# Optimization experiments

Measured on AMD Instinct MI355X. Metric: run time of the kernel, lower is better.

## Reference

```python
import jax, jax.numpy as jnp
import numpy as np

B = 16384      # batch size
D = 512        # state_dim (= number of graph nodes)
HID = 512      # hidden_dim of main GCN blocks
EH = 32        # hidden dim of ENSO GCN blocks
K = 2          # fourier_modes
OMEGA = 2.0 * np.pi / 12.0


def setup_inputs() -> dict:
    ks = jax.random.split(jax.random.key(0), 20)
    def w(k, shape, scale=0.05):
        return (jax.random.normal(k, shape) * scale).astype(jnp.float32)
    inp = {
        "x": jax.random.normal(ks[0], (B, D), dtype=jnp.float32),
        "t": jax.random.uniform(ks[1], (1,), dtype=jnp.float32) * 12.0,
        "fourier_coeffs": w(ks[2], (D, D, 2 * K + 1), 0.1),
        # quadratic_graph: GCN(D->HID) -> ReLU -> GCN(HID->D)
        "quad_W1": w(ks[3], (D, HID)), "quad_b1": jnp.zeros((HID,), jnp.float32),
        "quad_W2": w(ks[4], (HID, D)), "quad_b2": jnp.zeros((D,), jnp.float32),
        # cubic_graph
        "cubic_W1": w(ks[5], (D, HID)), "cubic_b1": jnp.zeros((HID,), jnp.float32),
        "cubic_W2": w(ks[6], (HID, D)), "cubic_b2": jnp.zeros((D,), jnp.float32),
        # enso_T_graph: GCN(5->32) -> ReLU -> GCN(32->1)
        "ensoT_W1": w(ks[7], (5, EH)), "ensoT_b1": jnp.zeros((EH,), jnp.float32),
        "ensoT_W2": w(ks[8], (EH, 1)), "ensoT_b2": jnp.zeros((1,), jnp.float32),
        # enso_H_graph
        "ensoH_W1": w(ks[9], (5, EH)), "ensoH_b1": jnp.zeros((EH,), jnp.float32),
        "ensoH_W2": w(ks[10], (EH, 1)), "ensoH_b2": jnp.zeros((1,), jnp.float32),
    }
    return inp


def _gcn2(feat, W1, b1, W2, b2):
    # Fully-connected graph + self-loops => normalized adjacency P = (1/N) 11^T.
    # All node rows are identical (x expanded over nodes), so P @ X == X and every
    # node's output is identical: the 2-layer GCN collapses to two dense GEMMs.
    h = jax.nn.relu(feat @ W1 + b1)
    return h @ W2 + b2


def reference(x, t, fourier_coeffs,
              quad_W1, quad_b1, quad_W2, quad_b2,
              cubic_W1, cubic_b1, cubic_W2, cubic_b2,
              ensoT_W1, ensoT_b1, ensoT_W2, ensoT_b2,
              ensoH_W1, ensoH_b1, ensoH_W2, ensoH_b2):
    ts = t[0]
    # --- Seasonal linear operator L(t) = C0 + sum_k Ck^c cos(k w t) + Ck^s sin(k w t)
    L = fourier_coeffs[:, :, 0]
    for k in range(1, K + 1):
        L = L + fourier_coeffs[:, :, 2 * k - 1] * jnp.cos(k * OMEGA * ts)
        L = L + fourier_coeffs[:, :, 2 * k] * jnp.sin(k * OMEGA * ts)
    linear_term = jnp.einsum('ij,bj->bi', L, x)  # [B, D]

    # --- Graph nonlinear terms (per-node outputs identical; mean over feature dim)
    quad = _gcn2(x, quad_W1, quad_b1, quad_W2, quad_b2)        # [B, D]
    cubic = _gcn2(x, cubic_W1, cubic_b1, cubic_W2, cubic_b2)   # [B, D]
    # torch: out[node] identical for all nodes; .mean(dim=1) over features -> same
    # scalar replicated across the state dimension.
    quad_terms = jnp.broadcast_to(quad.mean(axis=1, keepdims=True), (x.shape[0], D))
    cubic_terms = jnp.broadcast_to(cubic.mean(axis=1, keepdims=True), (x.shape[0], D))
    nonlinear = quad_terms + cubic_terms

    # --- ENSO-specific physics (state_dim >= 2)
    T = x[:, 0:1]
    H = x[:, 1:2]
    fT = jnp.concatenate([T, H, T * T, T * H, T * T * T], axis=1)   # [B, 5]
    fH = jnp.concatenate([T, H, T * T, T * H, T * H * H], axis=1)   # [B, 5]
    cT = _gcn2(fT, ensoT_W1, ensoT_b1, ensoT_W2, ensoT_b2)  # [B, 1]
    cH = _gcn2(fH, ensoH_W1, ensoH_b1, ensoH_W2, ensoH_b2)  # [B, 1]
    pad = jnp.zeros((x.shape[0], D - 2), dtype=x.dtype)
    nonlinear = nonlinear + jnp.concatenate([cT, cH, pad], axis=1)

    return linear_term + nonlinear
```

## Files before the change

kernel.cpp:

```cpp
#include <hip/hip_runtime.h>


#define OMEGA_F 0.5235987755982988f

typedef __attribute__((ext_vector_type(8))) short short8;
typedef __attribute__((ext_vector_type(4))) float f32x4;

__device__ __forceinline__ unsigned short f2bf(float f) {
  union { float f; unsigned int u; } a;
  a.f = f;
  unsigned int u = a.u;
  return (unsigned short)((u + 0x7fffu + ((u >> 16) & 1u)) >> 16);
}

__global__ void build_wcat(const float* __restrict__ fc, const float* __restrict__ qW1,
                           const float* __restrict__ cW1, const float* __restrict__ t,
                           unsigned short* __restrict__ WT) {
  int idx = blockIdx.x * 256 + threadIdx.x;
  int n = idx >> 9;
  int k = idx & 511;
  float v;
  if (n < 512) {
    float th = OMEGA_F * t[0];
    float s1, c1, s2, c2;
    sincosf(th, &s1, &c1);
    sincosf(2.0f * th, &s2, &c2);
    const float* p = fc + ((size_t)n * 512 + k) * 5;
    v = p[0] + p[1] * c1 + p[2] * s1 + p[3] * c2 + p[4] * s2;
  } else if (n < 1024) {
    v = qW1[(size_t)k * 512 + (n - 512)];
  } else {
    v = cW1[(size_t)k * 512 + (n - 1024)];
  }
  WT[idx] = f2bf(v);
}

__global__ void build_means(const float* __restrict__ qW2, const float* __restrict__ cW2,
                            const float* __restrict__ qb2, const float* __restrict__ cb2,
                            float* __restrict__ qw2m, float* __restrict__ cw2m,
                            float* __restrict__ b2m) {
  int b = blockIdx.x, tdx = threadIdx.x;
  if (b < 4) {
    const float* W = (b < 2) ? qW2 : cW2;
    float* o = (b < 2) ? qw2m : cw2m;
    int h = (b & 1) * 256 + tdx;
    const float4* row = (const float4*)(W + (size_t)h * 512);
    float s = 0.f;
    for (int i = 0; i < 128; ++i) { float4 v = row[i]; s += (v.x + v.y) + (v.z + v.w); }
    o[h] = s * (1.0f / 512.0f);
  } else {
    __shared__ float sm[256];
    sm[tdx] = qb2[tdx] + qb2[tdx + 256];
    __syncthreads();
    for (int w = 128; w > 0; w >>= 1) { if (tdx < w) sm[tdx] += sm[tdx + w]; __syncthreads(); }
    if (tdx == 0) b2m[0] = sm[0] * (1.0f / 512.0f);
    __syncthreads();
    sm[tdx] = cb2[tdx] + cb2[tdx + 256];
    __syncthreads();
    for (int w = 128; w > 0; w >>= 1) { if (tdx < w) sm[tdx] += sm[tdx + w]; __syncthreads(); }
    if (tdx == 0) b2m[1] = sm[0] * (1.0f / 512.0f);
  }
}

__global__ void enso_kernel(const float* __restrict__ x,
                            const float* __restrict__ tW1, const float* __restrict__ tb1,
                            const float* __restrict__ tW2, const float* __restrict__ tb2,
                            const float* __restrict__ hW1, const float* __restrict__ hb1,
                            const float* __restrict__ hW2, const float* __restrict__ hb2,
                            float* __restrict__ cT, float* __restrict__ cH) {
  int b = blockIdx.x * 256 + threadIdx.x;
  float T = x[(size_t)b * 512];
  float H = x[(size_t)b * 512 + 1];
  float fT[5] = {T, H, T * T, T * H, T * T * T};
  float fH[5] = {T, H, T * T, T * H, T * H * H};
  float sT = tb2[0], sH = hb2[0];
#pragma unroll 4
  for (int e = 0; e < 32; ++e) {
    float a1 = tb1[e], a2 = hb1[e];
#pragma unroll
    for (int f = 0; f < 5; ++f) {
      a1 += fT[f] * tW1[f * 32 + e];
      a2 += fH[f] * hW1[f * 32 + e];
    }
    sT += fmaxf(a1, 0.f) * tW2[e];
    sH += fmaxf(a2, 0.f) * hW2[e];
  }
  cT[b] = sT;
  cH[b] = sH;
}

__global__ void convert_x(const float4* __restrict__ x, uint2* __restrict__ xb) {
  int i = blockIdx.x * 256 + threadIdx.x;
  float4 v = x[i];
  uint2 r;
  r.x = (unsigned)f2bf(v.x) | ((unsigned)f2bf(v.y) << 16);
  r.y = (unsigned)f2bf(v.z) | ((unsigned)f2bf(v.w) << 16);
  xb[i] = r;
}

__global__ __launch_bounds__(256) void gemm_kernel(
    const unsigned short* __restrict__ A,
    const unsigned short* __restrict__ Bt,
    const float* __restrict__ qb1, const float* __restrict__ cb1,
    const float* __restrict__ qw2m, const float* __restrict__ cw2m,
    float* __restrict__ out, float* __restrict__ rowadd) {
  __shared__ unsigned short As[128 * 32];
  __shared__ unsigned short Bs[128 * 32];
  const int tid = threadIdx.x;
  const int lane = tid & 63;
  const int wave = tid >> 6;
  const int wm = wave & 1;
  const int wn = wave >> 1;
  const int m_base = blockIdx.x * 128;
  const int n_base = blockIdx.y * 128;
  const int lrow = lane & 15;
  const int lk = (lane >> 4) * 8;

  f32x4 acc[4][4];
#pragma unroll
  for (int i = 0; i < 4; ++i)
#pragma unroll
    for (int j = 0; j < 4; ++j) acc[i][j] = (f32x4){0.f, 0.f, 0.f, 0.f};

  for (int k0 = 0; k0 < 512; k0 += 32) {
#pragma unroll
    for (int u = 0; u < 2; ++u) {
      int f = tid + u * 256;
      int row = f >> 2;
      int cg = (f & 3) * 8;
      *(uint4*)(&As[row * 32 + cg]) =
          *(const uint4*)(&A[(size_t)(m_base + row) * 512 + k0 + cg]);
      *(uint4*)(&Bs[row * 32 + cg]) =
          *(const uint4*)(&Bt[(size_t)(n_base + row) * 512 + k0 + cg]);
    }
    __syncthreads();
    short8 af[4], bfr[4];
#pragma unroll
    for (int i = 0; i < 4; ++i)
      af[i] = *(const short8*)(&As[(wm * 64 + i * 16 + lrow) * 32 + lk]);
#pragma unroll
    for (int j = 0; j < 4; ++j)
      bfr[j] = *(const short8*)(&Bs[(wn * 64 + j * 16 + lrow) * 32 + lk]);
#pragma unroll
    for (int i = 0; i < 4; ++i)
#pragma unroll
      for (int j = 0; j < 4; ++j)
        acc[i][j] = __builtin_amdgcn_mfma_f32_16x16x32_bf16(af[i], bfr[j], acc[i][j], 0, 0, 0);
    __syncthreads();
  }

  const int rbase = m_base + wm * 64 + (lane >> 4) * 4;
  if (blockIdx.y < 4) {
#pragma unroll
    for (int i = 0; i < 4; ++i)
#pragma unroll
      for (int j = 0; j < 4; ++j) {
        int col = n_base + wn * 64 + j * 16 + lrow;
#pragma unroll
        for (int r = 0; r < 4; ++r)
          out[(size_t)(rbase + i * 16 + r) * 512 + col] = acc[i][j][r];
      }
  } else {
    const bool isq = (blockIdx.y < 8);
    const float* b1 = isq ? qb1 : cb1;
    const float* w2m = isq ? qw2m : cw2m;
    const int cb0 = n_base - (isq ? 512 : 1024) + wn * 64 + lrow;
    float rs[4][4];
#pragma unroll
    for (int i = 0; i < 4; ++i)
#pragma unroll
      for (int r = 0; r < 4; ++r) rs[i][r] = 0.f;
#pragma unroll
    for (int j = 0; j < 4; ++j) {
      int col = cb0 + j * 16;
      float bb = b1[col];
      float ww = w2m[col];
#pragma unroll
      for (int i = 0; i < 4; ++i)
#pragma unroll
        for (int r = 0; r < 4; ++r)
          rs[i][r] += fmaxf(acc[i][j][r] + bb, 0.f) * ww;
    }
#pragma unroll
    for (int i = 0; i < 4; ++i)
#pragma unroll
      for (int r = 0; r < 4; ++r) {
        float v = rs[i][r];
        v += __shfl_xor(v, 1, 64);
        v += __shfl_xor(v, 2, 64);
        v += __shfl_xor(v, 4, 64);
        v += __shfl_xor(v, 8, 64);
        if (lrow == 0) atomicAdd(&rowadd[rbase + i * 16 + r], v);
      }
  }
}

__global__ void finalize(float* __restrict__ out, const float* __restrict__ rowadd,
                         const float* __restrict__ b2m, const float* __restrict__ cT,
                         const float* __restrict__ cH) {
  int idx = blockIdx.x * 256 + threadIdx.x;
  int row = idx >> 7;
  int c4 = idx & 127;
  float add = rowadd[row] + b2m[0] + b2m[1];
  float4 v = ((float4*)out)[idx];
  v.x += add; v.y += add; v.z += add; v.w += add;
  if (c4 == 0) { v.x += cT[row]; v.y += cH[row]; }
  ((float4*)out)[idx] = v;
}

extern "C" void kernel_launch(void* const* d_in, const int* in_sizes, int n_in,
                              void* d_out, int out_size, void* d_ws, size_t ws_size,
                              hipStream_t stream) {
  const float* x   = (const float*)d_in[0];
  const float* t   = (const float*)d_in[1];
  const float* fc  = (const float*)d_in[2];
  const float* qW1 = (const float*)d_in[3];
  const float* qb1 = (const float*)d_in[4];
  const float* qW2 = (const float*)d_in[5];
  const float* qb2 = (const float*)d_in[6];
  const float* cW1 = (const float*)d_in[7];
  const float* cb1 = (const float*)d_in[8];
  const float* cW2 = (const float*)d_in[9];
  const float* cb2 = (const float*)d_in[10];
  const float* tW1 = (const float*)d_in[11];
  const float* tb1 = (const float*)d_in[12];
  const float* tW2 = (const float*)d_in[13];
  const float* tb2 = (const float*)d_in[14];
  const float* hW1 = (const float*)d_in[15];
  const float* hb1 = (const float*)d_in[16];
  const float* hW2 = (const float*)d_in[17];
  const float* hb2 = (const float*)d_in[18];
  float* out = (float*)d_out;

  char* ws = (char*)d_ws;
  unsigned short* WT = (unsigned short*)(ws);
  unsigned short* xb = (unsigned short*)(ws + 1572864);
  float* qw2m   = (float*)(ws + 18350080);
  float* cw2m   = (float*)(ws + 18352128);
  float* b2m    = (float*)(ws + 18354176);
  float* cT     = (float*)(ws + 18354432);
  float* cH     = (float*)(ws + 18419968);
  float* rowadd = (float*)(ws + 18485504);

  hipMemsetAsync(rowadd, 0, 16384 * sizeof(float), stream);
  build_wcat<<<3072, 256, 0, stream>>>(fc, qW1, cW1, t, WT);
  build_means<<<5, 256, 0, stream>>>(qW2, cW2, qb2, cb2, qw2m, cw2m, b2m);
  enso_kernel<<<64, 256, 0, stream>>>(x, tW1, tb1, tW2, tb2, hW1, hb1, hW2, hb2, cT, cH);
  convert_x<<<8192, 256, 0, stream>>>((const float4*)x, (uint2*)xb);
  gemm_kernel<<<dim3(128, 12), 256, 0, stream>>>(xb, WT, qb1, cb1, qw2m, cw2m, out, rowadd);
  finalize<<<8192, 256, 0, stream>>>(out, rowadd, b2m, cT, cH);
}
```

Baseline: 202.7 us.

## Split GEMM into nonlinear and linear passes and fuse finalize into epilogue

Merges the small prep kernels (weight build, means, memset, enso, x conversion) into two launches. The single GEMM becomes a nonlinear GEMM that accumulates row sums first, then a linear GEMM whose epilogue adds those row sums, the biases and the ENSO terms before writing the output. This removes the separate finalize pass, which re-read and re-wrote the full output. The GEMM tile loads now use global_load_lds direct-to-LDS copies instead of going through registers. The cost is two GEMM launches in sequence instead of one, so the linear GEMM cannot overlap with the nonlinear one.

```diff
diff --git a/kernel.cpp b/kernel.cpp
--- a/kernel.cpp
+++ b/kernel.cpp
@@ -13,37 +13,43 @@
   return (unsigned short)((u + 0x7fffu + ((u >> 16) & 1u)) >> 16);
 }
 
-__global__ void build_wcat(const float* __restrict__ fc, const float* __restrict__ qW1,
-                           const float* __restrict__ cW1, const float* __restrict__ t,
-                           unsigned short* __restrict__ WT) {
-  int idx = blockIdx.x * 256 + threadIdx.x;
-  int n = idx >> 9;
-  int k = idx & 511;
-  float v;
-  if (n < 512) {
-    float th = OMEGA_F * t[0];
-    float s1, c1, s2, c2;
-    sincosf(th, &s1, &c1);
-    sincosf(2.0f * th, &s2, &c2);
-    const float* p = fc + ((size_t)n * 512 + k) * 5;
-    v = p[0] + p[1] * c1 + p[2] * s1 + p[3] * c2 + p[4] * s2;
-  } else if (n < 1024) {
-    v = qW1[(size_t)k * 512 + (n - 512)];
-  } else {
-    v = cW1[(size_t)k * 512 + (n - 1024)];
-  }
-  WT[idx] = f2bf(v);
-}
-
-__global__ void build_means(const float* __restrict__ qW2, const float* __restrict__ cW2,
+__device__ __forceinline__ void gload16(const void* g, void* l) {
+  __builtin_amdgcn_global_load_lds(
+      (const __attribute__((address_space(1))) unsigned int*)g,
+      (__attribute__((address_space(3))) unsigned int*)l, 16, 0, 0);
+}
+
+__global__ void prep_kernel(const float* __restrict__ fc, const float* __restrict__ qW1,
+                            const float* __restrict__ cW1, const float* __restrict__ t,
+                            const float* __restrict__ qW2, const float* __restrict__ cW2,
                             const float* __restrict__ qb2, const float* __restrict__ cb2,
+                            unsigned short* __restrict__ WT,
                             float* __restrict__ qw2m, float* __restrict__ cw2m,
                             float* __restrict__ b2m) {
   int b = blockIdx.x, tdx = threadIdx.x;
-  if (b < 4) {
-    const float* W = (b < 2) ? qW2 : cW2;
-    float* o = (b < 2) ? qw2m : cw2m;
-    int h = (b & 1) * 256 + tdx;
+  if (b < 3072) {
+    int idx = b * 256 + tdx;
+    int n = idx >> 9;
+    int k = idx & 511;
+    float v;
+    if (n < 512) {
+      float th = OMEGA_F * t[0];
+      float s1, c1, s2, c2;
+      sincosf(th, &s1, &c1);
+      sincosf(2.0f * th, &s2, &c2);
+      const float* p = fc + ((size_t)n * 512 + k) * 5;
+      v = p[0] + p[1] * c1 + p[2] * s1 + p[3] * c2 + p[4] * s2;
+    } else if (n < 1024) {
+      v = qW1[(size_t)k * 512 + (n - 512)];
+    } else {
+      v = cW1[(size_t)k * 512 + (n - 1024)];
+    }
+    WT[idx] = f2bf(v);
+  } else if (b < 3076) {
+    int bb = b - 3072;
+    const float* W = (bb < 2) ? qW2 : cW2;
+    float* o = (bb < 2) ? qw2m : cw2m;
+    int h = (bb & 1) * 256 + tdx;
     const float4* row = (const float4*)(W + (size_t)h * 512);
     float s = 0.f;
     for (int i = 0; i < 128; ++i) { float4 v = row[i]; s += (v.x + v.y) + (v.z + v.w); }
@@ -62,150 +68,160 @@
   }
 }
 
-__global__ void enso_kernel(const float* __restrict__ x,
-                            const float* __restrict__ tW1, const float* __restrict__ tb1,
-                            const float* __restrict__ tW2, const float* __restrict__ tb2,
-                            const float* __restrict__ hW1, const float* __restrict__ hb1,
-                            const float* __restrict__ hW2, const float* __restrict__ hb2,
-                            float* __restrict__ cT, float* __restrict__ cH) {
-  int b = blockIdx.x * 256 + threadIdx.x;
-  float T = x[(size_t)b * 512];
-  float H = x[(size_t)b * 512 + 1];
-  float fT[5] = {T, H, T * T, T * H, T * T * T};
-  float fH[5] = {T, H, T * T, T * H, T * H * H};
-  float sT = tb2[0], sH = hb2[0];
+__global__ void conv_enso(const float4* __restrict__ x4, uint2* __restrict__ xb,
+                          const float* __restrict__ x,
+                          const float* __restrict__ tW1, const float* __restrict__ tb1,
+                          const float* __restrict__ tW2, const float* __restrict__ tb2,
+                          const float* __restrict__ hW1, const float* __restrict__ hb1,
+                          const float* __restrict__ hW2, const float* __restrict__ hb2,
+                          float* __restrict__ cT, float* __restrict__ cH,
+                          float* __restrict__ rowadd) {
+  int b = blockIdx.x;
+  if (b < 8192) {
+    int i = b * 256 + threadIdx.x;
+    float4 v = x4[i];
+    uint2 r;
+    r.x = (unsigned)f2bf(v.x) | ((unsigned)f2bf(v.y) << 16);
+    r.y = (unsigned)f2bf(v.z) | ((unsigned)f2bf(v.w) << 16);
+    xb[i] = r;
+  } else {
+    int row = (b - 8192) * 256 + threadIdx.x;
+    rowadd[row] = 0.f;
+    float T = x[(size_t)row * 512];
+    float H = x[(size_t)row * 512 + 1];
+    float fT[5] = {T, H, T * T, T * H, T * T * T};
+    float fH[5] = {T, H, T * T, T * H, T * H * H};
+    float sT = tb2[0], sH = hb2[0];
 #pragma unroll 4
-  for (int e = 0; e < 32; ++e) {
-    float a1 = tb1[e], a2 = hb1[e];
-#pragma unroll
-    for (int f = 0; f < 5; ++f) {
-      a1 += fT[f] * tW1[f * 32 + e];
-      a2 += fH[f] * hW1[f * 32 + e];
+    for (int e = 0; e < 32; ++e) {
+      float a1 = tb1[e], a2 = hb1[e];
+#pragma unroll
+      for (int f = 0; f < 5; ++f) {
+        a1 += fT[f] * tW1[f * 32 + e];
+        a2 += fH[f] * hW1[f * 32 + e];
+      }
+      sT += fmaxf(a1, 0.f) * tW2[e];
+      sH += fmaxf(a2, 0.f) * hW2[e];
     }
-    sT += fmaxf(a1, 0.f) * tW2[e];
-    sH += fmaxf(a2, 0.f) * hW2[e];
-  }
-  cT[b] = sT;
-  cH[b] = sH;
-}
-
-__global__ void convert_x(const float4* __restrict__ x, uint2* __restrict__ xb) {
-  int i = blockIdx.x * 256 + threadIdx.x;
-  float4 v = x[i];
-  uint2 r;
-  r.x = (unsigned)f2bf(v.x) | ((unsigned)f2bf(v.y) << 16);
-  r.y = (unsigned)f2bf(v.z) | ((unsigned)f2bf(v.w) << 16);
-  xb[i] = r;
-}
-
-__global__ __launch_bounds__(256) void gemm_kernel(
+    cT[row] = sT;
+    cH[row] = sH;
+  }
+}
+
+#define GEMM_MAINLOOP(A_, Bt_)                                                    \
+  __shared__ unsigned short As[128 * 32];                                         \
+  __shared__ unsigned short Bs[128 * 32];                                         \
+  const int tid = threadIdx.x;                                                    \
+  const int lane = tid & 63;                                                      \
+  const int wave = tid >> 6;                                                      \
+  const int wm = wave & 1;                                                        \
+  const int wn = wave >> 1;                                                       \
+  const int m_base = blockIdx.x * 128;                                            \
+  const int n_base = blockIdx.y * 128;                                            \
+  const int lrow = lane & 15;                                                     \
+  const int lk = (lane >> 4) * 8;                                                 \
+  const int sr0 = wave * 16 + (lane >> 2);                                        \
+  const int scg = (lane & 3) * 8;                                                 \
+  const unsigned short* gA0 = A_ + (size_t)(m_base + sr0) * 512 + scg;            \
+  const unsigned short* gA1 = gA0 + 64 * 512;                                     \
+  const unsigned short* gB0 = Bt_ + (size_t)(n_base + sr0) * 512 + scg;           \
+  const unsigned short* gB1 = gB0 + 64 * 512;                                     \
+  unsigned short* lA0 = As + wave * 512;                                          \
+  unsigned short* lA1 = As + (wave + 4) * 512;                                    \
+  unsigned short* lB0 = Bs + wave * 512;                                          \
+  unsigned short* lB1 = Bs + (wave + 4) * 512;                                    \
+  f32x4 acc[4][4];                                                                \
+  _Pragma("unroll") for (int i = 0; i < 4; ++i)                                   \
+      _Pragma("unroll") for (int j = 0; j < 4; ++j)                               \
+          acc[i][j] = (f32x4){0.f, 0.f, 0.f, 0.f};                                \
+  for (int k0 = 0; k0 < 512; k0 += 32) {                                          \
+    gload16(gA0, lA0);                                                            \
+    gload16(gA1, lA1);                                                            \
+    gload16(gB0, lB0);                                                            \
+    gload16(gB1, lB1);                                                            \
+    gA0 += 32; gA1 += 32; gB0 += 32; gB1 += 32;                                   \
+    __syncthreads();                                                              \
+    short8 af[4], bfr[4];                                                         \
+    _Pragma("unroll") for (int i = 0; i < 4; ++i)                                 \
+        af[i] = *(const short8*)(&As[(wm * 64 + i * 16 + lrow) * 32 + lk]);       \
+    _Pragma("unroll") for (int j = 0; j < 4; ++j)                                 \
+        bfr[j] = *(const short8*)(&Bs[(wn * 64 + j * 16 + lrow) * 32 + lk]);      \
+    _Pragma("unroll") for (int i = 0; i < 4; ++i)                                 \
+        _Pragma("unroll") for (int j = 0; j < 4; ++j)                             \
+            acc[i][j] = __builtin_amdgcn_mfma_f32_16x16x32_bf16(af[i], bfr[j],    \
+                                                                acc[i][j], 0, 0, 0); \
+    __syncthreads();                                                              \
+  }
+
+__global__ __launch_bounds__(256) void nl_gemm(
     const unsigned short* __restrict__ A,
     const unsigned short* __restrict__ Bt,
     const float* __restrict__ qb1, const float* __restrict__ cb1,
     const float* __restrict__ qw2m, const float* __restrict__ cw2m,
-    float* __restrict__ out, float* __restrict__ rowadd) {
-  __shared__ unsigned short As[128 * 32];
-  __shared__ unsigned short Bs[128 * 32];
-  const int tid = threadIdx.x;
-  const int lane = tid & 63;
-  const int wave = tid >> 6;
-  const int wm = wave & 1;
-  const int wn = wave >> 1;
-  const int m_base = blockIdx.x * 128;
-  const int n_base = blockIdx.y * 128;
-  const int lrow = lane & 15;
-  const int lk = (lane >> 4) * 8;
-
-  f32x4 acc[4][4];
+    float* __restrict__ rowadd) {
+  GEMM_MAINLOOP(A, Bt)
+  const int rbase = m_base + wm * 64 + (lane >> 4) * 4;
+  const bool isq = (blockIdx.y < 4);
+  const float* b1 = isq ? qb1 : cb1;
+  const float* w2m = isq ? qw2m : cw2m;
+  const int cb0 = (isq ? n_base : n_base - 512) + wn * 64 + lrow;
+  float rs[4][4];
 #pragma unroll
   for (int i = 0; i < 4; ++i)
 #pragma unroll
-    for (int j = 0; j < 4; ++j) acc[i][j] = (f32x4){0.f, 0.f, 0.f, 0.f};
-
-  for (int k0 = 0; k0 < 512; k0 += 32) {
-#pragma unroll
-    for (int u = 0; u < 2; ++u) {
-      int f = tid + u * 256;
-      int row = f >> 2;
-      int cg = (f & 3) * 8;
-      *(uint4*)(&As[row * 32 + cg]) =
-          *(const uint4*)(&A[(size_t)(m_base + row) * 512 + k0 + cg]);
-      *(uint4*)(&Bs[row * 32 + cg]) =
-          *(const uint4*)(&Bt[(size_t)(n_base + row) * 512 + k0 + cg]);
+    for (int r = 0; r < 4; ++r) rs[i][r] = 0.f;
+#pragma unroll
+  for (int j = 0; j < 4; ++j) {
+    int col = cb0 + j * 16;
+    float bb = b1[col];
+    float ww = w2m[col];
+#pragma unroll
+    for (int i = 0; i < 4; ++i)
+#pragma unroll
+      for (int r = 0; r < 4; ++r)
+        rs[i][r] += fmaxf(acc[i][j][r] + bb, 0.f) * ww;
+  }
+#pragma unroll
+  for (int i = 0; i < 4; ++i)
+#pragma unroll
+    for (int r = 0; r < 4; ++r) {
+      float v = rs[i][r];
+      v += __shfl_xor(v, 1, 64);
+      v += __shfl_xor(v, 2, 64);
+      v += __shfl_xor(v, 4, 64);
+      v += __shfl_xor(v, 8, 64);
+      if (lrow == 0) atomicAdd(&rowadd[rbase + i * 16 + r], v);
     }
-    __syncthreads();
-    short8 af[4], bfr[4];
+}
+
+__global__ __launch_bounds__(256) void lin_gemm(
+    const unsigned short* __restrict__ A,
+    const unsigned short* __restrict__ Bt,
+    const float* __restrict__ rowadd, const float* __restrict__ b2m,
+    const float* __restrict__ cT, const float* __restrict__ cH,
+    float* __restrict__ out) {
+  GEMM_MAINLOOP(A, Bt)
+  const int rbase = m_base + wm * 64 + (lane >> 4) * 4;
+  const float b2s = b2m[0] + b2m[1];
+  float ra[4][4];
+#pragma unroll
+  for (int i = 0; i < 4; ++i)
+#pragma unroll
+    for (int r = 0; r < 4; ++r) ra[i][r] = rowadd[rbase + i * 16 + r] + b2s;
+#pragma unroll
+  for (int j = 0; j < 4; ++j) {
+    int col = n_base + wn * 64 + j * 16 + lrow;
 #pragma unroll
     for (int i = 0; i < 4; ++i)
-      af[i] = *(const short8*)(&As[(wm * 64 + i * 16 + lrow) * 32 + lk]);
-#pragma unroll
-    for (int j = 0; j < 4; ++j)
-      bfr[j] = *(const short8*)(&Bs[(wn * 64 + j * 16 + lrow) * 32 + lk]);
-#pragma unroll
-    for (int i = 0; i < 4; ++i)
-#pragma unroll
-      for (int j = 0; j < 4; ++j)
-        acc[i][j] = __builtin_amdgcn_mfma_f32_16x16x32_bf16(af[i], bfr[j], acc[i][j], 0, 0, 0);
-    __syncthreads();
-  }
-
-  const int rbase = m_base + wm * 64 + (lane >> 4) * 4;
-  if (blockIdx.y < 4) {
-#pragma unroll
-    for (int i = 0; i < 4; ++i)
-#pragma unroll
-      for (int j = 0; j < 4; ++j) {
-        int col = n_base + wn * 64 + j * 16 + lrow;
-#pragma unroll
-        for (int r = 0; r < 4; ++r)
-          out[(size_t)(rbase + i * 16 + r) * 512 + col] = acc[i][j][r];
+#pragma unroll
+      for (int r = 0; r < 4; ++r) {
+        int row = rbase + i * 16 + r;
+        float v = acc[i][j][r] + ra[i][r];
+        if (col == 0) v += cT[row];
+        if (col == 1) v += cH[row];
+        out[(size_t)row * 512 + col] = v;
       }
-  } else {
-    const bool isq = (blockIdx.y < 8);
-    const float* b1 = isq ? qb1 : cb1;
-    const float* w2m = isq ? qw2m : cw2m;
-    const int cb0 = n_base - (isq ? 512 : 1024) + wn * 64 + lrow;
-    float rs[4][4];
-#pragma unroll
-    for (int i = 0; i < 4; ++i)
-#pragma unroll
-      for (int r = 0; r < 4; ++r) rs[i][r] = 0.f;
-#pragma unroll
-    for (int j = 0; j < 4; ++j) {
-      int col = cb0 + j * 16;
-      float bb = b1[col];
-      float ww = w2m[col];
-#pragma unroll
-      for (int i = 0; i < 4; ++i)
-#pragma unroll
-        for (int r = 0; r < 4; ++r)
-          rs[i][r] += fmaxf(acc[i][j][r] + bb, 0.f) * ww;
-    }
-#pragma unroll
-    for (int i = 0; i < 4; ++i)
-#pragma unroll
-      for (int r = 0; r < 4; ++r) {
-        float v = rs[i][r];
-        v += __shfl_xor(v, 1, 64);
-        v += __shfl_xor(v, 2, 64);
-        v += __shfl_xor(v, 4, 64);
-        v += __shfl_xor(v, 8, 64);
-        if (lrow == 0) atomicAdd(&rowadd[rbase + i * 16 + r], v);
-      }
-  }
-}
-
-__global__ void finalize(float* __restrict__ out, const float* __restrict__ rowadd,
-                         const float* __restrict__ b2m, const float* __restrict__ cT,
-                         const float* __restrict__ cH) {
-  int idx = blockIdx.x * 256 + threadIdx.x;
-  int row = idx >> 7;
-  int c4 = idx & 127;
-  float add = rowadd[row] + b2m[0] + b2m[1];
-  float4 v = ((float4*)out)[idx];
-  v.x += add; v.y += add; v.z += add; v.w += add;
-  if (c4 == 0) { v.x += cT[row]; v.y += cH[row]; }
-  ((float4*)out)[idx] = v;
+  }
 }
 
 extern "C" void kernel_launch(void* const* d_in, const int* in_sizes, int n_in,
@@ -242,11 +258,12 @@
   float* cH     = (float*)(ws + 18419968);
   float* rowadd = (float*)(ws + 18485504);
 
-  hipMemsetAsync(rowadd, 0, 16384 * sizeof(float), stream);
-  build_wcat<<<3072, 256, 0, stream>>>(fc, qW1, cW1, t, WT);
-  build_means<<<5, 256, 0, stream>>>(qW2, cW2, qb2, cb2, qw2m, cw2m, b2m);
-  enso_kernel<<<64, 256, 0, stream>>>(x, tW1, tb1, tW2, tb2, hW1, hb1, hW2, hb2, cT, cH);
-  convert_x<<<8192, 256, 0, stream>>>((const float4*)x, (uint2*)xb);
-  gemm_kernel<<<dim3(128, 12), 256, 0, stream>>>(xb, WT, qb1, cb1, qw2m, cw2m, out, rowadd);
-  finalize<<<8192, 256, 0, stream>>>(out, rowadd, b2m, cT, cH);
-}
+  prep_kernel<<<3077, 256, 0, stream>>>(fc, qW1, cW1, t, qW2, cW2, qb2, cb2,
+                                        WT, qw2m, cw2m, b2m);
+  conv_enso<<<8256, 256, 0, stream>>>((const float4*)x, (uint2*)xb, x,
+                                      tW1, tb1, tW2, tb2, hW1, hb1, hW2, hb2,
+                                      cT, cH, rowadd);
+  nl_gemm<<<dim3(128, 8), 256, 0, stream>>>(xb, WT + (size_t)512 * 512,
+                                            qb1, cb1, qw2m, cw2m, rowadd);
+  lin_gemm<<<dim3(128, 4), 256, 0, stream>>>(xb, WT, rowadd, b2m, cT, cH, out);
+}
```

Result: faster. 188.5 us (-7.0%).

## Fuse prep kernels and finalize into GEMM with per-row-block counter sync

Applied to the files above, without the earlier changes.

Merges the weight build, mean, ENSO, x-conversion and rowadd-zeroing kernels into a single prep launch, which also replaces the separate memset. The GEMM kernel now computes the hidden-layer reductions first and signals a per-row-block counter. Half of the blocks then compute the linear tile, spin until all eight hidden contributions for their rows are in, and write the final output with the bias and ENSO terms added. This removes the separate finalize pass that read and wrote the whole output again. GEMM tiles are also loaded straight from global memory into LDS. The spin-wait depends on every block being resident at once, so it carries a deadlock risk if they are not.

```diff
diff --git a/kernel.cpp b/kernel.cpp
--- a/kernel.cpp
+++ b/kernel.cpp
@@ -13,42 +13,56 @@
   return (unsigned short)((u + 0x7fffu + ((u >> 16) & 1u)) >> 16);
 }
 
-__global__ void build_wcat(const float* __restrict__ fc, const float* __restrict__ qW1,
-                           const float* __restrict__ cW1, const float* __restrict__ t,
-                           unsigned short* __restrict__ WT) {
-  int idx = blockIdx.x * 256 + threadIdx.x;
-  int n = idx >> 9;
-  int k = idx & 511;
-  float v;
-  if (n < 512) {
-    float th = OMEGA_F * t[0];
-    float s1, c1, s2, c2;
-    sincosf(th, &s1, &c1);
-    sincosf(2.0f * th, &s2, &c2);
-    const float* p = fc + ((size_t)n * 512 + k) * 5;
-    v = p[0] + p[1] * c1 + p[2] * s1 + p[3] * c2 + p[4] * s2;
-  } else if (n < 1024) {
-    v = qW1[(size_t)k * 512 + (n - 512)];
-  } else {
-    v = cW1[(size_t)k * 512 + (n - 1024)];
-  }
-  WT[idx] = f2bf(v);
-}
-
-__global__ void build_means(const float* __restrict__ qW2, const float* __restrict__ cW2,
-                            const float* __restrict__ qb2, const float* __restrict__ cb2,
-                            float* __restrict__ qw2m, float* __restrict__ cw2m,
-                            float* __restrict__ b2m) {
+__device__ __forceinline__ void gload16(const void* g, void* l) {
+  __builtin_amdgcn_global_load_lds(
+      (const __attribute__((address_space(1))) unsigned int*)g,
+      (__attribute__((address_space(3))) unsigned int*)l, 16, 0, 0);
+}
+
+__global__ void prep_conv(const float* __restrict__ fc, const float* __restrict__ qW1,
+                          const float* __restrict__ cW1, const float* __restrict__ t,
+                          const float* __restrict__ qW2, const float* __restrict__ cW2,
+                          const float* __restrict__ qb2, const float* __restrict__ cb2,
+                          const float4* __restrict__ x4, const float* __restrict__ x,
+                          const float* __restrict__ tW1, const float* __restrict__ tb1,
+                          const float* __restrict__ tW2, const float* __restrict__ tb2,
+                          const float* __restrict__ hW1, const float* __restrict__ hb1,
+                          const float* __restrict__ hW2, const float* __restrict__ hb2,
+                          unsigned short* __restrict__ WT, uint2* __restrict__ xb,
+                          float* __restrict__ qw2m, float* __restrict__ cw2m,
+                          float* __restrict__ b2m, float* __restrict__ cT,
+                          float* __restrict__ cH, float* __restrict__ rowadd,
+                          int* __restrict__ cnt) {
   int b = blockIdx.x, tdx = threadIdx.x;
-  if (b < 4) {
-    const float* W = (b < 2) ? qW2 : cW2;
-    float* o = (b < 2) ? qw2m : cw2m;
-    int h = (b & 1) * 256 + tdx;
+  if (b < 3072) {
+    int idx = b * 256 + tdx;
+    int n = idx >> 9;
+    int k = idx & 511;
+    float v;
+    if (n < 512) {
+      float th = OMEGA_F * t[0];
+      float s1, c1, s2, c2;
+      sincosf(th, &s1, &c1);
+      sincosf(2.0f * th, &s2, &c2);
+      const float* p = fc + ((size_t)n * 512 + k) * 5;
+      v = p[0] + p[1] * c1 + p[2] * s1 + p[3] * c2 + p[4] * s2;
+    } else if (n < 1024) {
+      v = qW1[(size_t)k * 512 + (n - 512)];
+    } else {
+      v = cW1[(size_t)k * 512 + (n - 1024)];
+    }
+    WT[idx] = f2bf(v);
+  } else if (b < 3076) {
+    int bb = b - 3072;
+    const float* W = (bb < 2) ? qW2 : cW2;
+    float* o = (bb < 2) ? qw2m : cw2m;
+    int h = (bb & 1) * 256 + tdx;
     const float4* row = (const float4*)(W + (size_t)h * 512);
     float s = 0.f;
     for (int i = 0; i < 128; ++i) { float4 v = row[i]; s += (v.x + v.y) + (v.z + v.w); }
     o[h] = s * (1.0f / 512.0f);
-  } else {
+  } else if (b == 3076) {
+    if (tdx < 128) cnt[tdx] = 0;
     __shared__ float sm[256];
     sm[tdx] = qb2[tdx] + qb2[tdx + 256];
     __syncthreads();
@@ -59,51 +73,86 @@
     __syncthreads();
     for (int w = 128; w > 0; w >>= 1) { if (tdx < w) sm[tdx] += sm[tdx + w]; __syncthreads(); }
     if (tdx == 0) b2m[1] = sm[0] * (1.0f / 512.0f);
-  }
-}
-
-__global__ void enso_kernel(const float* __restrict__ x,
-                            const float* __restrict__ tW1, const float* __restrict__ tb1,
-                            const float* __restrict__ tW2, const float* __restrict__ tb2,
-                            const float* __restrict__ hW1, const float* __restrict__ hb1,
-                            const float* __restrict__ hW2, const float* __restrict__ hb2,
-                            float* __restrict__ cT, float* __restrict__ cH) {
-  int b = blockIdx.x * 256 + threadIdx.x;
-  float T = x[(size_t)b * 512];
-  float H = x[(size_t)b * 512 + 1];
-  float fT[5] = {T, H, T * T, T * H, T * T * T};
-  float fH[5] = {T, H, T * T, T * H, T * H * H};
-  float sT = tb2[0], sH = hb2[0];
+  } else if (b < 3077 + 8192) {
+    int i = (b - 3077) * 256 + tdx;
+    float4 v = x4[i];
+    uint2 r;
+    r.x = (unsigned)f2bf(v.x) | ((unsigned)f2bf(v.y) << 16);
+    r.y = (unsigned)f2bf(v.z) | ((unsigned)f2bf(v.w) << 16);
+    xb[i] = r;
+  } else {
+    int row = (b - 11269) * 256 + tdx;
+    rowadd[row] = 0.f;
+    float T = x[(size_t)row * 512];
+    float H = x[(size_t)row * 512 + 1];
+    float fT[5] = {T, H, T * T, T * H, T * T * T};
+    float fH[5] = {T, H, T * T, T * H, T * H * H};
+    float sT = tb2[0], sH = hb2[0];
 #pragma unroll 4
-  for (int e = 0; e < 32; ++e) {
-    float a1 = tb1[e], a2 = hb1[e];
-#pragma unroll
-    for (int f = 0; f < 5; ++f) {
-      a1 += fT[f] * tW1[f * 32 + e];
-      a2 += fH[f] * hW1[f * 32 + e];
-    }
-    sT += fmaxf(a1, 0.f) * tW2[e];
-    sH += fmaxf(a2, 0.f) * hW2[e];
-  }
-  cT[b] = sT;
-  cH[b] = sH;
-}
-
-__global__ void convert_x(const float4* __restrict__ x, uint2* __restrict__ xb) {
-  int i = blockIdx.x * 256 + threadIdx.x;
-  float4 v = x[i];
-  uint2 r;
-  r.x = (unsigned)f2bf(v.x) | ((unsigned)f2bf(v.y) << 16);
-  r.y = (unsigned)f2bf(v.z) | ((unsigned)f2bf(v.w) << 16);
-  xb[i] = r;
-}
-
-__global__ __launch_bounds__(256) void gemm_kernel(
+    for (int e = 0; e < 32; ++e) {
+      float a1 = tb1[e], a2 = hb1[e];
+#pragma unroll
+      for (int f = 0; f < 5; ++f) {
+        a1 += fT[f] * tW1[f * 32 + e];
+        a2 += fH[f] * hW1[f * 32 + e];
+      }
+      sT += fmaxf(a1, 0.f) * tW2[e];
+      sH += fmaxf(a2, 0.f) * hW2[e];
+    }
+    cT[row] = sT;
+    cH[row] = sH;
+  }
+}
+
+__device__ __forceinline__ void mainloop(const unsigned short* __restrict__ gA,
+                                         const unsigned short* __restrict__ gB,
+                                         unsigned short* __restrict__ As,
+                                         unsigned short* __restrict__ Bs,
+                                         int wave, int wm, int wn, int lrow, int lk,
+                                         f32x4 acc[4][4]) {
+  const unsigned short* gA0 = gA;
+  const unsigned short* gA1 = gA + 64 * 512;
+  const unsigned short* gB0 = gB;
+  const unsigned short* gB1 = gB + 64 * 512;
+  unsigned short* lA0 = As + wave * 512;
+  unsigned short* lA1 = As + (wave + 4) * 512;
+  unsigned short* lB0 = Bs + wave * 512;
+  unsigned short* lB1 = Bs + (wave + 4) * 512;
+#pragma unroll
+  for (int i = 0; i < 4; ++i)
+#pragma unroll
+    for (int j = 0; j < 4; ++j) acc[i][j] = (f32x4){0.f, 0.f, 0.f, 0.f};
+  for (int k0 = 0; k0 < 512; k0 += 32) {
+    gload16(gA0, lA0);
+    gload16(gA1, lA1);
+    gload16(gB0, lB0);
+    gload16(gB1, lB1);
+    gA0 += 32; gA1 += 32; gB0 += 32; gB1 += 32;
+    __syncthreads();
+    short8 af[4], bfr[4];
+#pragma unroll
+    for (int i = 0; i < 4; ++i)
+      af[i] = *(const short8*)(&As[(wm * 64 + i * 16 + lrow) * 32 + lk]);
+#pragma unroll
+    for (int j = 0; j < 4; ++j)
+      bfr[j] = *(const short8*)(&Bs[(wn * 64 + j * 16 + lrow) * 32 + lk]);
+#pragma unroll
+    for (int i = 0; i < 4; ++i)
+#pragma unroll
+      for (int j = 0; j < 4; ++j)
+        acc[i][j] = __builtin_amdgcn_mfma_f32_16x16x32_bf16(af[i], bfr[j], acc[i][j], 0, 0, 0);
+    __syncthreads();
+  }
+}
+
+__global__ __launch_bounds__(256, 4) void mega_gemm(
     const unsigned short* __restrict__ A,
-    const unsigned short* __restrict__ Bt,
+    const unsigned short* __restrict__ WT,
     const float* __restrict__ qb1, const float* __restrict__ cb1,
     const float* __restrict__ qw2m, const float* __restrict__ cw2m,
-    float* __restrict__ out, float* __restrict__ rowadd) {
+    const float* __restrict__ b2m, const float* __restrict__ cT,
+    const float* __restrict__ cH, float* __restrict__ rowadd,
+    int* __restrict__ cnt, float* __restrict__ out) {
   __shared__ unsigned short As[128 * 32];
   __shared__ unsigned short Bs[128 * 32];
   const int tid = threadIdx.x;
@@ -111,60 +160,27 @@
   const int wave = tid >> 6;
   const int wm = wave & 1;
   const int wn = wave >> 1;
-  const int m_base = blockIdx.x * 128;
-  const int n_base = blockIdx.y * 128;
+  const int bx = blockIdx.x;
+  const int by = blockIdx.y;
+  const int m_base = bx * 128;
   const int lrow = lane & 15;
   const int lk = (lane >> 4) * 8;
+  const int sr0 = wave * 16 + (lane >> 2);
+  const int scg = (lane & 3) * 8;
+  const unsigned short* gA = A + (size_t)(m_base + sr0) * 512 + scg;
+  const int rbase = m_base + wm * 64 + (lane >> 4) * 4;
 
   f32x4 acc[4][4];
-#pragma unroll
-  for (int i = 0; i < 4; ++i)
-#pragma unroll
-    for (int j = 0; j < 4; ++j) acc[i][j] = (f32x4){0.f, 0.f, 0.f, 0.f};
-
-  for (int k0 = 0; k0 < 512; k0 += 32) {
-#pragma unroll
-    for (int u = 0; u < 2; ++u) {
-      int f = tid + u * 256;
-      int row = f >> 2;
-      int cg = (f & 3) * 8;
-      *(uint4*)(&As[row * 32 + cg]) =
-          *(const uint4*)(&A[(size_t)(m_base + row) * 512 + k0 + cg]);
-      *(uint4*)(&Bs[row * 32 + cg]) =
-          *(const uint4*)(&Bt[(size_t)(n_base + row) * 512 + k0 + cg]);
-    }
-    __syncthreads();
-    short8 af[4], bfr[4];
-#pragma unroll
-    for (int i = 0; i < 4; ++i)
-      af[i] = *(const short8*)(&As[(wm * 64 + i * 16 + lrow) * 32 + lk]);
-#pragma unroll
-    for (int j = 0; j < 4; ++j)
-      bfr[j] = *(const short8*)(&Bs[(wn * 64 + j * 16 + lrow) * 32 + lk]);
-#pragma unroll
-    for (int i = 0; i < 4; ++i)
-#pragma unroll
-      for (int j = 0; j < 4; ++j)
-        acc[i][j] = __builtin_amdgcn_mfma_f32_16x16x32_bf16(af[i], bfr[j], acc[i][j], 0, 0, 0);
-    __syncthreads();
-  }
-
-  const int rbase = m_base + wm * 64 + (lane >> 4) * 4;
-  if (blockIdx.y < 4) {
-#pragma unroll
-    for (int i = 0; i < 4; ++i)
-#pragma unroll
-      for (int j = 0; j < 4; ++j) {
-        int col = n_base + wn * 64 + j * 16 + lrow;
-#pragma unroll
-        for (int r = 0; r < 4; ++r)
-          out[(size_t)(rbase + i * 16 + r) * 512 + col] = acc[i][j][r];
-      }
-  } else {
-    const bool isq = (blockIdx.y < 8);
+
+  {
+    const int n_base = by * 128;
+    const unsigned short* BtN = WT + (size_t)512 * 512;
+    mainloop(gA, BtN + (size_t)(n_base + sr0) * 512 + scg, As, Bs,
+             wave, wm, wn, lrow, lk, acc);
+    const bool isq = (by < 4);
     const float* b1 = isq ? qb1 : cb1;
     const float* w2m = isq ? qw2m : cw2m;
-    const int cb0 = n_base - (isq ? 512 : 1024) + wn * 64 + lrow;
+    const int cb0 = (isq ? n_base : n_base - 512) + wn * 64 + lrow;
     float rs[4][4];
 #pragma unroll
     for (int i = 0; i < 4; ++i)
@@ -193,19 +209,44 @@
         if (lrow == 0) atomicAdd(&rowadd[rbase + i * 16 + r], v);
       }
   }
-}
-
-__global__ void finalize(float* __restrict__ out, const float* __restrict__ rowadd,
-                         const float* __restrict__ b2m, const float* __restrict__ cT,
-                         const float* __restrict__ cH) {
-  int idx = blockIdx.x * 256 + threadIdx.x;
-  int row = idx >> 7;
-  int c4 = idx & 127;
-  float add = rowadd[row] + b2m[0] + b2m[1];
-  float4 v = ((float4*)out)[idx];
-  v.x += add; v.y += add; v.z += add; v.w += add;
-  if (c4 == 0) { v.x += cT[row]; v.y += cH[row]; }
-  ((float4*)out)[idx] = v;
+  __syncthreads();
+  if (tid == 0) {
+    __threadfence();
+    __hip_atomic_fetch_add(&cnt[bx], 1, __ATOMIC_RELEASE, __HIP_MEMORY_SCOPE_AGENT);
+  }
+
+  if (((bx + by) & 1) == 1) {
+    const int n_base = (by >> 1) * 128;
+    mainloop(gA, WT + (size_t)(n_base + sr0) * 512 + scg, As, Bs,
+             wave, wm, wn, lrow, lk, acc);
+    if (tid == 0) {
+      while (__hip_atomic_load(&cnt[bx], __ATOMIC_ACQUIRE, __HIP_MEMORY_SCOPE_AGENT) < 8)
+        __builtin_amdgcn_s_sleep(2);
+    }
+    __syncthreads();
+    const float b2s = b2m[0] + b2m[1];
+    float ra[4][4];
+#pragma unroll
+    for (int i = 0; i < 4; ++i)
+#pragma unroll
+      for (int r = 0; r < 4; ++r)
+        ra[i][r] = __hip_atomic_load(&rowadd[rbase + i * 16 + r], __ATOMIC_RELAXED,
+                                     __HIP_MEMORY_SCOPE_AGENT) + b2s;
+#pragma unroll
+    for (int j = 0; j < 4; ++j) {
+      int col = n_base + wn * 64 + j * 16 + lrow;
+#pragma unroll
+      for (int i = 0; i < 4; ++i)
+#pragma unroll
+        for (int r = 0; r < 4; ++r) {
+          int row = rbase + i * 16 + r;
+          float v = acc[i][j][r] + ra[i][r];
+          if (col == 0) v += cT[row];
+          if (col == 1) v += cH[row];
+          out[(size_t)row * 512 + col] = v;
+        }
+    }
+  }
 }
 
 extern "C" void kernel_launch(void* const* d_in, const int* in_sizes, int n_in,
@@ -241,12 +282,13 @@
   float* cT     = (float*)(ws + 18354432);
   float* cH     = (float*)(ws + 18419968);
   float* rowadd = (float*)(ws + 18485504);
-
-  hipMemsetAsync(rowadd, 0, 16384 * sizeof(float), stream);
-  build_wcat<<<3072, 256, 0, stream>>>(fc, qW1, cW1, t, WT);
-  build_means<<<5, 256, 0, stream>>>(qW2, cW2, qb2, cb2, qw2m, cw2m, b2m);
-  enso_kernel<<<64, 256, 0, stream>>>(x, tW1, tb1, tW2, tb2, hW1, hb1, hW2, hb2, cT, cH);
-  convert_x<<<8192, 256, 0, stream>>>((const float4*)x, (uint2*)xb);
-  gemm_kernel<<<dim3(128, 12), 256, 0, stream>>>(xb, WT, qb1, cb1, qw2m, cw2m, out, rowadd);
-  finalize<<<8192, 256, 0, stream>>>(out, rowadd, b2m, cT, cH);
-}
+  int*   cnt    = (int*)(ws + 18551040);
+
+  prep_conv<<<11333, 256, 0, stream>>>(fc, qW1, cW1, t, qW2, cW2, qb2, cb2,
+                                       (const float4*)x, x,
+                                       tW1, tb1, tW2, tb2, hW1, hb1, hW2, hb2,
+                                       WT, (uint2*)xb, qw2m, cw2m, b2m, cT, cH,
+                                       rowadd, cnt);
+  mega_gemm<<<dim3(128, 8), 256, 0, stream>>>(xb, WT, qb1, cb1, qw2m, cw2m,
+                                              b2m, cT, cH, rowadd, cnt, out);
+}
```

Result: slower. 213.3 us (+5.2%).
